# Performance work log

Hardware: AMD Instinct MI355X
Metric: run time of the kernel (lower is better)

The kernel has to match this reference:

```python
import jax, jax.numpy as jnp
import numpy as np
import math


def gen_slopes(n_heads, alibi_bias_max=1.0):
    # matches torch gen_slopes: _n_heads = next pow2, m = arange(1.._n)*max/_n, slopes = 2^-m
    _n = 2 ** math.ceil(math.log2(n_heads))
    m = jnp.arange(1, _n + 1, dtype=jnp.float32) * (alibi_bias_max / _n)
    slopes = 1.0 / jnp.power(2.0, m)
    if _n != n_heads:
        slopes = jnp.concatenate([slopes[1::2], slopes[::2]])[:n_heads]
    return slopes.reshape(1, n_heads, 1, 1)


def build_alibi_bias(n_heads, seq_len, alibi_bias_max=1.0):
    # full=False branch: bias over key positions only, shape [1, H, 1, L]
    pos = jnp.arange(1 - seq_len, 1, dtype=jnp.float32).reshape(1, 1, 1, seq_len)
    return pos * gen_slopes(n_heads, alibi_bias_max)


def setup_inputs() -> dict:
    key = jax.random.key(0)
    kq, kk, kv = jax.random.split(key, 3)
    B, L, H, E = 8, 1024, 8, 64
    return {
        "queries": jax.random.normal(kq, (B, L, H, E), dtype=jnp.float32),
        "keys": jax.random.normal(kk, (B, L, H, E), dtype=jnp.float32),
        "values": jax.random.normal(kv, (B, L, H, E), dtype=jnp.float32),
        "patch_index": -1,
    }


def reference(queries, keys, values, patch_index):
    B, L, H, E = queries.shape
    scale = 1.0 / math.sqrt(E)
    # scores: [B, H, L, L]
    scores = jnp.einsum('blhe,bshe->bhls', queries, keys)
    attn = scale * scores + build_alibi_bias(H, L)  # ALiBi bias, alibi_bias_max=1
    series = jax.nn.softmax(attn, axis=-1)  # dropout is identity in eval mode
    V = jnp.einsum('bhls,bshd->blhd', series, values)
    # patch_index == -1: identity branch, series unchanged
    return (V, series)
```

## Files before the change

kernel.cpp:

```cpp
#include <hip/hip_runtime.h>
#include <hip/hip_bf16.h>


typedef short short8 __attribute__((ext_vector_type(8)));
typedef short short4v __attribute__((ext_vector_type(4)));
typedef float f32x4 __attribute__((ext_vector_type(4)));
typedef unsigned short u16x4 __attribute__((ext_vector_type(4)));

#define B_ 8
#define L_ 1024
#define H_ 8
#define E_ 64
#define RSTRIDE (H_ * E_)
#define QBLK 64
#define CHUNK 64
#define NCH (L_ / CHUNK)
#define CHUNK_USH (CHUNK * E_)

__device__ __forceinline__ unsigned short f2bf(float f) {
  return __builtin_bit_cast(unsigned short, __float2bfloat16(f));
}
__device__ __forceinline__ short8 ldfrag(const float* p) {
  float4 a = *reinterpret_cast<const float4*>(p);
  float4 b = *reinterpret_cast<const float4*>(p + 4);
  return (short8){(short)f2bf(a.x), (short)f2bf(a.y), (short)f2bf(a.z),
                  (short)f2bf(a.w), (short)f2bf(b.x), (short)f2bf(b.y),
                  (short)f2bf(b.z), (short)f2bf(b.w)};
}

__device__ __forceinline__ f32x4 mfma16(short4v a, short4v b, f32x4 c) {
#if __has_builtin(__builtin_amdgcn_mfma_f32_16x16x16bf16_1k)
  return __builtin_amdgcn_mfma_f32_16x16x16bf16_1k(a, b, c, 0, 0, 0);
#else
  asm volatile(
      "s_nop 1\n\t"
      "v_mfma_f32_16x16x16_bf16 %0, %1, %2, %0\n\t"
      "s_nop 2"
      : "+v"(c)
      : "v"(a), "v"(b));
  return c;
#endif
}

__device__ __forceinline__ void gld16(const unsigned short* g,
                                      unsigned short* l) {
  __builtin_amdgcn_global_load_lds(
      (const __attribute__((address_space(1))) unsigned int*)g,
      (__attribute__((address_space(3))) unsigned int*)l, 16, 0, 0);
}

#define BAR_VM(N)                                         \
  {                                                       \
    asm volatile("s_waitcnt vmcnt(" #N ")" ::: "memory"); \
    __builtin_amdgcn_s_barrier();                         \
    __builtin_amdgcn_sched_barrier(0);                    \
  }

__global__ __launch_bounds__(256, 4) void prep_kv(
    const float* __restrict__ Kg, const float* __restrict__ Vg,
    unsigned short* __restrict__ Kbf, unsigned short* __restrict__ VTbf) {
  __shared__ unsigned short vt[64 * 64];

  const int t = threadIdx.x;
  const int id = blockIdx.x;
  const int bh = id & 63;
  const int sc = id >> 6;
  const int h = bh & 7, b = bh >> 3;
  const int s0 = sc * CHUNK;

  const float* Kb = Kg + ((size_t)b * L_ + s0) * RSTRIDE + h * E_;
  const float* Vb = Vg + ((size_t)b * L_ + s0) * RSTRIDE + h * E_;
  unsigned short* Ko = Kbf + (size_t)(bh * NCH + sc) * CHUNK_USH;
  unsigned short* Vo = VTbf + (size_t)(bh * NCH + sc) * CHUNK_USH;

#pragma unroll
  for (int i = 0; i < 2; ++i) {
    const int j = t + 256 * i;
    const int s = j >> 3;
    const int e8 = (j & 7) ^ (s & 7);
    const float* kp = Kb + (size_t)s * RSTRIDE + 8 * e8;
    float4 a = *reinterpret_cast<const float4*>(kp);
    float4 c = *reinterpret_cast<const float4*>(kp + 4);
    *reinterpret_cast<u16x4*>(&Ko[j * 8]) =
        (u16x4){f2bf(a.x), f2bf(a.y), f2bf(a.z), f2bf(a.w)};
    *reinterpret_cast<u16x4*>(&Ko[j * 8 + 4]) =
        (u16x4){f2bf(c.x), f2bf(c.y), f2bf(c.z), f2bf(c.w)};
  }
  {
    const int e = t & 63, w = t >> 6;
#pragma unroll
    for (int i = 0; i < 4; ++i) {
      const int s4 = 4 * w + 16 * i;
      const float* vp = Vb + (size_t)s4 * RSTRIDE + e;
      u16x4 u = {f2bf(vp[0]), f2bf(vp[RSTRIDE]), f2bf(vp[2 * RSTRIDE]),
                 f2bf(vp[3 * RSTRIDE])};
      *reinterpret_cast<u16x4*>(
          &vt[e * 64 + (((s4 >> 3) ^ (e & 7)) << 3) + (s4 & 7)]) = u;
    }
  }
  __syncthreads();
#pragma unroll
  for (int i = 0; i < 2; ++i) {
    const int j = t + 256 * i;
    u16x4 u0 = *reinterpret_cast<const u16x4*>(&vt[j * 8]);
    u16x4 u1 = *reinterpret_cast<const u16x4*>(&vt[j * 8 + 4]);
    *reinterpret_cast<u16x4*>(&Vo[j * 8]) = u0;
    *reinterpret_cast<u16x4*>(&Vo[j * 8 + 4]) = u1;
  }
}

__global__ __launch_bounds__(256, 4) void alibi_attn(
    const float* __restrict__ Qg, const unsigned short* __restrict__ Kbf,
    const unsigned short* __restrict__ VTbf, float* __restrict__ Vout,
    float* __restrict__ Pout) {
  __shared__ unsigned short sBuf[4][CHUNK_USH];

  const int t = threadIdx.x;
  const int lane = t & 63;
  const int w = t >> 6;
  const int col = lane & 15;
  const int kg = lane >> 4;

  const int id = blockIdx.x;
  const int qb = id >> 6;
  const int bh = id & 63;
  const int h = bh & 7;
  const int b = bh >> 3;
  const int q0 = qb * QBLK;

  const float sc_l2e = 0.125f * 1.44269504f;
  const float sl_l2e = exp2f(-(float)(h + 1) * 0.125f) * 1.44269504f;

  const unsigned short* Kc = Kbf + (size_t)bh * NCH * CHUNK_USH;
  const unsigned short* Vc = VTbf + (size_t)bh * NCH * CHUNK_USH;

  short8 qf0, qf1;
  {
    const float* qp =
        Qg + ((size_t)b * L_ + q0 + 16 * w + col) * RSTRIDE + h * E_ + 8 * kg;
    qf0 = ldfrag(qp);
    qf1 = ldfrag(qp + 32);
  }

  const float kbias0 = sl_l2e * (float)(4 * kg - 1023) - 32.0f;

#define STAGE(srcbase, c, dst)                                       \
  {                                                                  \
    const unsigned short* src = (srcbase) + (size_t)(c)*CHUNK_USH;   \
    _Pragma("unroll") for (int i = 0; i < 2; ++i) {                  \
      const int seg = i * 4 + w;                                     \
      gld16(src + (size_t)(seg * 64 + lane) * 8, (dst) + seg * 512); \
    }                                                                \
  }
#define PIN() __builtin_amdgcn_sched_barrier(0)

  float z0 = 0.f, z1 = 0.f, z2 = 0.f, z3 = 0.f;
  STAGE(Kc, 0, sBuf[0]);
  STAGE(Kc, 1, sBuf[1]);
  PIN();
  BAR_VM(2);
  for (int c = 0; c < NCH; ++c) {
    if (c + 2 < NCH) {
      STAGE(Kc, c + 2, sBuf[(c + 2) & 3]);
      PIN();
    }
    const unsigned short* kb = sBuf[c & 3];
#pragma unroll
    for (int kt = 0; kt < 4; ++kt) {
      const int row = 16 * kt + col;
      short8 k0 = *reinterpret_cast<const short8*>(
          &kb[row * 64 + ((kg ^ (row & 7)) << 3)]);
      short8 k1 = *reinterpret_cast<const short8*>(
          &kb[row * 64 + (((kg + 4) ^ (row & 7)) << 3)]);
      f32x4 acc = {0.f, 0.f, 0.f, 0.f};
      acc = __builtin_amdgcn_mfma_f32_16x16x32_bf16(k0, qf0, acc, 0, 0, 0);
      acc = __builtin_amdgcn_mfma_f32_16x16x32_bf16(k1, qf1, acc, 0, 0, 0);
      const float base = fmaf((float)(CHUNK * c + 16 * kt), sl_l2e, kbias0);
      z0 += __builtin_amdgcn_exp2f(fmaf(acc[0], sc_l2e, base));
      z1 += __builtin_amdgcn_exp2f(fmaf(acc[1], sc_l2e, base + sl_l2e));
      z2 += __builtin_amdgcn_exp2f(fmaf(acc[2], sc_l2e, base + 2.f * sl_l2e));
      z3 += __builtin_amdgcn_exp2f(fmaf(acc[3], sc_l2e, base + 3.f * sl_l2e));
    }
    if (c + 2 < NCH) {
      BAR_VM(2);
    } else {
      BAR_VM(0);
    }
  }
  float z = (z0 + z1) + (z2 + z3);
  z += __shfl_xor(z, 16, 64);
  z += __shfl_xor(z, 32, 64);
  const float minv = 1.0f / z;

  f32x4 oacc[4];
#pragma unroll
  for (int et = 0; et < 4; ++et) oacc[et] = (f32x4){0.f, 0.f, 0.f, 0.f};

  float* Pb =
      Pout + ((size_t)(b * H_ + h) * L_ + q0 + 16 * w + col) * L_ + 4 * kg;

  __syncthreads();
  STAGE(Kc, 0, sBuf[0]);
  STAGE(Vc, 0, sBuf[2]);
  PIN();
  BAR_VM(0);
  for (int c = 0; c < NCH; ++c) {
    if (c + 1 < NCH) {
      STAGE(Kc, c + 1, sBuf[(c + 1) & 1]);
      STAGE(Vc, c + 1, sBuf[2 + ((c + 1) & 1)]);
      PIN();
    }
    const unsigned short* kb = sBuf[c & 1];
    const unsigned short* vb = sBuf[2 + (c & 1)];
#pragma unroll
    for (int kt = 0; kt < 4; ++kt) {
      const int row = 16 * kt + col;
      short8 k0 = *reinterpret_cast<const short8*>(
          &kb[row * 64 + ((kg ^ (row & 7)) << 3)]);
      short8 k1 = *reinterpret_cast<const short8*>(
          &kb[row * 64 + (((kg + 4) ^ (row & 7)) << 3)]);
      f32x4 acc = {0.f, 0.f, 0.f, 0.f};
      acc = __builtin_amdgcn_mfma_f32_16x16x32_bf16(k0, qf0, acc, 0, 0, 0);
      acc = __builtin_amdgcn_mfma_f32_16x16x32_bf16(k1, qf1, acc, 0, 0, 0);
      short4v vf[4];
      const int g0 = 2 * kt + (kg >> 1);
      const int so = 4 * (kg & 1);
#pragma unroll
      for (int et = 0; et < 4; ++et) {
        const int e = 16 * et + col;
        vf[et] = *reinterpret_cast<const short4v*>(
            &vb[e * 64 + ((g0 ^ (e & 7)) << 3) + so]);
      }
      const float base = fmaf((float)(CHUNK * c + 16 * kt), sl_l2e, kbias0);
      f32x4 pf;
      pf[0] = __builtin_amdgcn_exp2f(fmaf(acc[0], sc_l2e, base)) * minv;
      pf[1] =
          __builtin_amdgcn_exp2f(fmaf(acc[1], sc_l2e, base + sl_l2e)) * minv;
      pf[2] = __builtin_amdgcn_exp2f(fmaf(acc[2], sc_l2e, base + 2.f * sl_l2e)) *
              minv;
      pf[3] = __builtin_amdgcn_exp2f(fmaf(acc[3], sc_l2e, base + 3.f * sl_l2e)) *
              minv;
      *reinterpret_cast<f32x4*>(Pb + CHUNK * c + 16 * kt) = pf;
      short4v pa = {(short)f2bf(pf[0]), (short)f2bf(pf[1]), (short)f2bf(pf[2]),
                    (short)f2bf(pf[3])};
#pragma unroll
      for (int et = 0; et < 4; ++et) oacc[et] = mfma16(pa, vf[et], oacc[et]);
    }
    BAR_VM(4);
  }

  float* Vo = Vout + (((size_t)b * L_ + q0 + 16 * w) * H_ + h) * E_;
#pragma unroll
  for (int et = 0; et < 4; ++et) {
#pragma unroll
    for (int r = 0; r < 4; ++r) {
      __builtin_nontemporal_store(oacc[et][r],
                                  &Vo[(4 * kg + r) * RSTRIDE + 16 * et + col]);
    }
  }
}

extern "C" void kernel_launch(void* const* d_in, const int* in_sizes, int n_in,
                              void* d_out, int out_size, void* d_ws,
                              size_t ws_size, hipStream_t stream) {
  const float* Q = (const float*)d_in[0];
  const float* K = (const float*)d_in[1];
  const float* V = (const float*)d_in[2];
  float* out = (float*)d_out;
  float* Vo = out;
  float* Po = out + (size_t)B_ * L_ * H_ * E_;
  unsigned short* Kbf = (unsigned short*)d_ws;
  unsigned short* VTbf = Kbf + (size_t)B_ * H_ * L_ * E_;
  hipLaunchKernelGGL(prep_kv, dim3(NCH * B_ * H_), dim3(256), 0, stream, K, V,
                     Kbf, VTbf);
  hipLaunchKernelGGL(alibi_attn, dim3((L_ / QBLK) * H_ * B_), dim3(256), 0,
                     stream, Q, Kbf, VTbf, Vo, Po);
}
```

Before: 95.36 us.

## Halve query block and key chunk size to two-wave workgroups

```diff
diff --git a/kernel.cpp b/kernel.cpp
--- a/kernel.cpp
+++ b/kernel.cpp
@@ -12,8 +12,8 @@
 #define H_ 8
 #define E_ 64
 #define RSTRIDE (H_ * E_)
-#define QBLK 64
-#define CHUNK 64
+#define QBLK 32
+#define CHUNK 32
 #define NCH (L_ / CHUNK)
 #define CHUNK_USH (CHUNK * E_)
 
@@ -55,47 +55,52 @@
     __builtin_amdgcn_s_barrier();                         \
     __builtin_amdgcn_sched_barrier(0);                    \
   }
+#define PIN() __builtin_amdgcn_sched_barrier(0)
 
 __global__ __launch_bounds__(256, 4) void prep_kv(
     const float* __restrict__ Kg, const float* __restrict__ Vg,
     unsigned short* __restrict__ Kbf, unsigned short* __restrict__ VTbf) {
-  __shared__ unsigned short vt[64 * 64];
+  __shared__ unsigned short vt[2 * CHUNK_USH];
 
   const int t = threadIdx.x;
   const int id = blockIdx.x;
   const int bh = id & 63;
   const int sc = id >> 6;
   const int h = bh & 7, b = bh >> 3;
-  const int s0 = sc * CHUNK;
+  const int s0 = sc * 64;
 
   const float* Kb = Kg + ((size_t)b * L_ + s0) * RSTRIDE + h * E_;
   const float* Vb = Vg + ((size_t)b * L_ + s0) * RSTRIDE + h * E_;
-  unsigned short* Ko = Kbf + (size_t)(bh * NCH + sc) * CHUNK_USH;
-  unsigned short* Vo = VTbf + (size_t)(bh * NCH + sc) * CHUNK_USH;
+  unsigned short* Ko = Kbf + (size_t)(bh * NCH + 2 * sc) * CHUNK_USH;
+  unsigned short* Vo = VTbf + (size_t)(bh * NCH + 2 * sc) * CHUNK_USH;
 
 #pragma unroll
   for (int i = 0; i < 2; ++i) {
     const int j = t + 256 * i;
-    const int s = j >> 3;
-    const int e8 = (j & 7) ^ (s & 7);
-    const float* kp = Kb + (size_t)s * RSTRIDE + 8 * e8;
+    const int ch = j >> 8;
+    const int jj = j & 255;
+    const int s = jj >> 3;
+    const int e8 = (jj & 7) ^ (s & 7);
+    const float* kp = Kb + (size_t)(32 * ch + s) * RSTRIDE + 8 * e8;
     float4 a = *reinterpret_cast<const float4*>(kp);
     float4 c = *reinterpret_cast<const float4*>(kp + 4);
-    *reinterpret_cast<u16x4*>(&Ko[j * 8]) =
+    *reinterpret_cast<u16x4*>(&Ko[(size_t)ch * CHUNK_USH + jj * 8]) =
         (u16x4){f2bf(a.x), f2bf(a.y), f2bf(a.z), f2bf(a.w)};
-    *reinterpret_cast<u16x4*>(&Ko[j * 8 + 4]) =
+    *reinterpret_cast<u16x4*>(&Ko[(size_t)ch * CHUNK_USH + jj * 8 + 4]) =
         (u16x4){f2bf(c.x), f2bf(c.y), f2bf(c.z), f2bf(c.w)};
   }
   {
-    const int e = t & 63, w = t >> 6;
+    const int e = t & 63, w4 = t >> 6;
 #pragma unroll
     for (int i = 0; i < 4; ++i) {
-      const int s4 = 4 * w + 16 * i;
+      const int s4 = 4 * w4 + 16 * i;
+      const int ch = s4 >> 5;
+      const int u = (s4 & 31) >> 2;
+      const int slot = u ^ (e & 7);
       const float* vp = Vb + (size_t)s4 * RSTRIDE + e;
-      u16x4 u = {f2bf(vp[0]), f2bf(vp[RSTRIDE]), f2bf(vp[2 * RSTRIDE]),
-                 f2bf(vp[3 * RSTRIDE])};
-      *reinterpret_cast<u16x4*>(
-          &vt[e * 64 + (((s4 >> 3) ^ (e & 7)) << 3) + (s4 & 7)]) = u;
+      u16x4 uv = {f2bf(vp[0]), f2bf(vp[RSTRIDE]), f2bf(vp[2 * RSTRIDE]),
+                  f2bf(vp[3 * RSTRIDE])};
+      *reinterpret_cast<u16x4*>(&vt[ch * CHUNK_USH + e * 32 + slot * 4]) = uv;
     }
   }
   __syncthreads();
@@ -109,7 +114,7 @@
   }
 }
 
-__global__ __launch_bounds__(256, 4) void alibi_attn(
+__global__ __launch_bounds__(128, 4) void alibi_attn(
     const float* __restrict__ Qg, const unsigned short* __restrict__ Kbf,
     const unsigned short* __restrict__ VTbf, float* __restrict__ Vout,
     float* __restrict__ Pout) {
@@ -148,11 +153,10 @@
   {                                                                  \
     const unsigned short* src = (srcbase) + (size_t)(c)*CHUNK_USH;   \
     _Pragma("unroll") for (int i = 0; i < 2; ++i) {                  \
-      const int seg = i * 4 + w;                                     \
+      const int seg = i * 2 + w;                                     \
       gld16(src + (size_t)(seg * 64 + lane) * 8, (dst) + seg * 512); \
     }                                                                \
   }
-#define PIN() __builtin_amdgcn_sched_barrier(0)
 
   float z0 = 0.f, z1 = 0.f, z2 = 0.f, z3 = 0.f;
   STAGE(Kc, 0, sBuf[0]);
@@ -166,7 +170,7 @@
     }
     const unsigned short* kb = sBuf[c & 3];
 #pragma unroll
-    for (int kt = 0; kt < 4; ++kt) {
+    for (int kt = 0; kt < 2; ++kt) {
       const int row = 16 * kt + col;
       short8 k0 = *reinterpret_cast<const short8*>(
           &kb[row * 64 + ((kg ^ (row & 7)) << 3)]);
@@ -213,7 +217,7 @@
     const unsigned short* kb = sBuf[c & 1];
     const unsigned short* vb = sBuf[2 + (c & 1)];
 #pragma unroll
-    for (int kt = 0; kt < 4; ++kt) {
+    for (int kt = 0; kt < 2; ++kt) {
       const int row = 16 * kt + col;
       short8 k0 = *reinterpret_cast<const short8*>(
           &kb[row * 64 + ((kg ^ (row & 7)) << 3)]);
@@ -223,13 +227,12 @@
       acc = __builtin_amdgcn_mfma_f32_16x16x32_bf16(k0, qf0, acc, 0, 0, 0);
       acc = __builtin_amdgcn_mfma_f32_16x16x32_bf16(k1, qf1, acc, 0, 0, 0);
       short4v vf[4];
-      const int g0 = 2 * kt + (kg >> 1);
-      const int so = 4 * (kg & 1);
 #pragma unroll
       for (int et = 0; et < 4; ++et) {
         const int e = 16 * et + col;
-        vf[et] = *reinterpret_cast<const short4v*>(
-            &vb[e * 64 + ((g0 ^ (e & 7)) << 3) + so]);
+        const int slot = (4 * kt + kg) ^ (e & 7);
+        vf[et] =
+            *reinterpret_cast<const short4v*>(&vb[e * 32 + slot * 4]);
       }
       const float base = fmaf((float)(CHUNK * c + 16 * kt), sl_l2e, kbias0);
       f32x4 pf;
@@ -246,7 +249,7 @@
 #pragma unroll
       for (int et = 0; et < 4; ++et) oacc[et] = mfma16(pa, vf[et], oacc[et]);
     }
-    BAR_VM(4);
+    BAR_VM(2);
   }
 
   float* Vo = Vout + (((size_t)b * L_ + q0 + 16 * w) * H_ + h) * E_;
@@ -271,8 +274,8 @@
   float* Po = out + (size_t)B_ * L_ * H_ * E_;
   unsigned short* Kbf = (unsigned short*)d_ws;
   unsigned short* VTbf = Kbf + (size_t)B_ * H_ * L_ * E_;
-  hipLaunchKernelGGL(prep_kv, dim3(NCH * B_ * H_), dim3(256), 0, stream, K, V,
+  hipLaunchKernelGGL(prep_kv, dim3(16 * B_ * H_), dim3(256), 0, stream, K, V,
                      Kbf, VTbf);
-  hipLaunchKernelGGL(alibi_attn, dim3((L_ / QBLK) * H_ * B_), dim3(256), 0,
+  hipLaunchKernelGGL(alibi_attn, dim3((L_ / QBLK) * H_ * B_), dim3(128), 0,
                      stream, Q, Kbf, VTbf, Vo, Po);
 }
```

Result: no change. 97.11 us (+1.8%).

## Fuse two-pass softmax into single pass with split-key waves and deferred normalization

Applied to the files above, without the earlier changes.

```diff
diff --git a/kernel.cpp b/kernel.cpp
--- a/kernel.cpp
+++ b/kernel.cpp
@@ -19,6 +19,9 @@
 
 __device__ __forceinline__ unsigned short f2bf(float f) {
   return __builtin_bit_cast(unsigned short, __float2bfloat16(f));
+}
+__device__ __forceinline__ float bf2f(unsigned int ubits) {
+  return __builtin_bit_cast(float, ubits << 16);
 }
 __device__ __forceinline__ short8 ldfrag(const float* p) {
   float4 a = *reinterpret_cast<const float4*>(p);
@@ -55,6 +58,7 @@
     __builtin_amdgcn_s_barrier();                         \
     __builtin_amdgcn_sched_barrier(0);                    \
   }
+#define PIN() __builtin_amdgcn_sched_barrier(0)
 
 __global__ __launch_bounds__(256, 4) void prep_kv(
     const float* __restrict__ Kg, const float* __restrict__ Vg,
@@ -109,15 +113,20 @@
   }
 }
 
-__global__ __launch_bounds__(256, 4) void alibi_attn(
+__global__ __launch_bounds__(512, 4) void alibi_attn(
     const float* __restrict__ Qg, const unsigned short* __restrict__ Kbf,
     const unsigned short* __restrict__ VTbf, float* __restrict__ Vout,
     float* __restrict__ Pout) {
-  __shared__ unsigned short sBuf[4][CHUNK_USH];
+  __shared__ unsigned short sK[2][2][CHUNK_USH];
+  __shared__ unsigned short sV[2][2][CHUNK_USH];
+  __shared__ float zbuf[2][4][16];
+  __shared__ float zinv[4][16];
 
   const int t = threadIdx.x;
   const int lane = t & 63;
   const int w = t >> 6;
+  const int qs = w & 3;
+  const int kh = w >> 2;
   const int col = lane & 15;
   const int kg = lane >> 4;
 
@@ -137,7 +146,7 @@
   short8 qf0, qf1;
   {
     const float* qp =
-        Qg + ((size_t)b * L_ + q0 + 16 * w + col) * RSTRIDE + h * E_ + 8 * kg;
+        Qg + ((size_t)b * L_ + q0 + 16 * qs + col) * RSTRIDE + h * E_ + 8 * kg;
     qf0 = ldfrag(qp);
     qf1 = ldfrag(qp + 32);
   }
@@ -148,23 +157,31 @@
   {                                                                  \
     const unsigned short* src = (srcbase) + (size_t)(c)*CHUNK_USH;   \
     _Pragma("unroll") for (int i = 0; i < 2; ++i) {                  \
-      const int seg = i * 4 + w;                                     \
+      const int seg = i * 4 + qs;                                    \
       gld16(src + (size_t)(seg * 64 + lane) * 8, (dst) + seg * 512); \
     }                                                                \
   }
-#define PIN() __builtin_amdgcn_sched_barrier(0)
-
-  float z0 = 0.f, z1 = 0.f, z2 = 0.f, z3 = 0.f;
-  STAGE(Kc, 0, sBuf[0]);
-  STAGE(Kc, 1, sBuf[1]);
+
+  float z0 = 0.f, z1 = 0.f;
+  f32x4 oacc[4];
+#pragma unroll
+  for (int et = 0; et < 4; ++et) oacc[et] = (f32x4){0.f, 0.f, 0.f, 0.f};
+  uint2 pw[8][4];
+
+  STAGE(Kc, 8 * kh, sK[kh][0]);
+  STAGE(Vc, 8 * kh, sV[kh][0]);
   PIN();
-  BAR_VM(2);
-  for (int c = 0; c < NCH; ++c) {
-    if (c + 2 < NCH) {
-      STAGE(Kc, c + 2, sBuf[(c + 2) & 3]);
+  BAR_VM(0);
+#pragma unroll
+  for (int c = 0; c < 8; ++c) {
+    if (c + 1 < 8) {
+      STAGE(Kc, 8 * kh + c + 1, sK[kh][(c + 1) & 1]);
+      STAGE(Vc, 8 * kh + c + 1, sV[kh][(c + 1) & 1]);
       PIN();
     }
-    const unsigned short* kb = sBuf[c & 3];
+    const int cc = 8 * kh + c;
+    const unsigned short* kb = sK[kh][c & 1];
+    const unsigned short* vb = sV[kh][c & 1];
 #pragma unroll
     for (int kt = 0; kt < 4; ++kt) {
       const int row = 16 * kt + col;
@@ -175,87 +192,83 @@
       f32x4 acc = {0.f, 0.f, 0.f, 0.f};
       acc = __builtin_amdgcn_mfma_f32_16x16x32_bf16(k0, qf0, acc, 0, 0, 0);
       acc = __builtin_amdgcn_mfma_f32_16x16x32_bf16(k1, qf1, acc, 0, 0, 0);
-      const float base = fmaf((float)(CHUNK * c + 16 * kt), sl_l2e, kbias0);
-      z0 += __builtin_amdgcn_exp2f(fmaf(acc[0], sc_l2e, base));
-      z1 += __builtin_amdgcn_exp2f(fmaf(acc[1], sc_l2e, base + sl_l2e));
-      z2 += __builtin_amdgcn_exp2f(fmaf(acc[2], sc_l2e, base + 2.f * sl_l2e));
-      z3 += __builtin_amdgcn_exp2f(fmaf(acc[3], sc_l2e, base + 3.f * sl_l2e));
-    }
-    if (c + 2 < NCH) {
-      BAR_VM(2);
-    } else {
-      BAR_VM(0);
-    }
-  }
-  float z = (z0 + z1) + (z2 + z3);
+      const float base = fmaf((float)(CHUNK * cc + 16 * kt), sl_l2e, kbias0);
+      float e0 = __builtin_amdgcn_exp2f(fmaf(acc[0], sc_l2e, base));
+      float e1 = __builtin_amdgcn_exp2f(fmaf(acc[1], sc_l2e, base + sl_l2e));
+      float e2 =
+          __builtin_amdgcn_exp2f(fmaf(acc[2], sc_l2e, base + 2.f * sl_l2e));
+      float e3 =
+          __builtin_amdgcn_exp2f(fmaf(acc[3], sc_l2e, base + 3.f * sl_l2e));
+      z0 += e0 + e1;
+      z1 += e2 + e3;
+      const unsigned int b0 = f2bf(e0), b1 = f2bf(e1);
+      const unsigned int b2 = f2bf(e2), b3 = f2bf(e3);
+      pw[c][kt] = make_uint2(b0 | (b1 << 16), b2 | (b3 << 16));
+      short4v pa = {(short)(unsigned short)b0, (short)(unsigned short)b1,
+                    (short)(unsigned short)b2, (short)(unsigned short)b3};
+#pragma unroll
+      for (int et = 0; et < 4; ++et) {
+        const int e = 16 * et + col;
+        const int g0 = 2 * kt + (kg >> 1);
+        short4v vf = *reinterpret_cast<const short4v*>(
+            &vb[e * 64 + ((g0 ^ (e & 7)) << 3) + 4 * (kg & 1)]);
+        oacc[et] = mfma16(pa, vf, oacc[et]);
+      }
+    }
+    BAR_VM(0);
+  }
+
+  float z = z0 + z1;
   z += __shfl_xor(z, 16, 64);
   z += __shfl_xor(z, 32, 64);
-  const float minv = 1.0f / z;
-
-  f32x4 oacc[4];
-#pragma unroll
-  for (int et = 0; et < 4; ++et) oacc[et] = (f32x4){0.f, 0.f, 0.f, 0.f};
-
-  float* Pb =
-      Pout + ((size_t)(b * H_ + h) * L_ + q0 + 16 * w + col) * L_ + 4 * kg;
-
+  if (kg == 0) zbuf[kh][qs][col] = z;
   __syncthreads();
-  STAGE(Kc, 0, sBuf[0]);
-  STAGE(Vc, 0, sBuf[2]);
-  PIN();
-  BAR_VM(0);
-  for (int c = 0; c < NCH; ++c) {
-    if (c + 1 < NCH) {
-      STAGE(Kc, c + 1, sBuf[(c + 1) & 1]);
-      STAGE(Vc, c + 1, sBuf[2 + ((c + 1) & 1)]);
-      PIN();
-    }
-    const unsigned short* kb = sBuf[c & 1];
-    const unsigned short* vb = sBuf[2 + (c & 1)];
+  const float minv = 1.0f / (zbuf[0][qs][col] + zbuf[1][qs][col]);
+
+  if (kh == 0 && kg == 0) zinv[qs][col] = minv;
+
+  float* obuf = reinterpret_cast<float*>(&sK[0][0][0]);
+  if (kh == 1) {
+#pragma unroll
+    for (int et = 0; et < 4; ++et)
+#pragma unroll
+      for (int r = 0; r < 4; ++r)
+        obuf[(qs * 16 + 4 * kg + r) * 64 + 16 * et + col] = oacc[et][r];
+  }
+  __syncthreads();
+  if (kh == 0) {
+    float minvR[4];
+#pragma unroll
+    for (int r = 0; r < 4; ++r) minvR[r] = zinv[qs][4 * kg + r];
+    float* Vo = Vout + (((size_t)b * L_ + q0 + 16 * qs) * H_ + h) * E_;
+#pragma unroll
+    for (int et = 0; et < 4; ++et) {
+#pragma unroll
+      for (int r = 0; r < 4; ++r) {
+        const float o =
+            (oacc[et][r] + obuf[(qs * 16 + 4 * kg + r) * 64 + 16 * et + col]) *
+            minvR[r];
+        __builtin_nontemporal_store(
+            o, &Vo[(4 * kg + r) * RSTRIDE + 16 * et + col]);
+      }
+    }
+  }
+
+  float* Pb = Pout + ((size_t)(b * H_ + h) * L_ + q0 + 16 * qs + col) * L_ +
+              4 * kg;
+#pragma unroll
+  for (int c = 0; c < 8; ++c) {
+    const int cc = 8 * kh + c;
 #pragma unroll
     for (int kt = 0; kt < 4; ++kt) {
-      const int row = 16 * kt + col;
-      short8 k0 = *reinterpret_cast<const short8*>(
-          &kb[row * 64 + ((kg ^ (row & 7)) << 3)]);
-      short8 k1 = *reinterpret_cast<const short8*>(
-          &kb[row * 64 + (((kg + 4) ^ (row & 7)) << 3)]);
-      f32x4 acc = {0.f, 0.f, 0.f, 0.f};
-      acc = __builtin_amdgcn_mfma_f32_16x16x32_bf16(k0, qf0, acc, 0, 0, 0);
-      acc = __builtin_amdgcn_mfma_f32_16x16x32_bf16(k1, qf1, acc, 0, 0, 0);
-      short4v vf[4];
-      const int g0 = 2 * kt + (kg >> 1);
-      const int so = 4 * (kg & 1);
-#pragma unroll
-      for (int et = 0; et < 4; ++et) {
-        const int e = 16 * et + col;
-        vf[et] = *reinterpret_cast<const short4v*>(
-            &vb[e * 64 + ((g0 ^ (e & 7)) << 3) + so]);
-      }
-      const float base = fmaf((float)(CHUNK * c + 16 * kt), sl_l2e, kbias0);
-      f32x4 pf;
-      pf[0] = __builtin_amdgcn_exp2f(fmaf(acc[0], sc_l2e, base)) * minv;
-      pf[1] =
-          __builtin_amdgcn_exp2f(fmaf(acc[1], sc_l2e, base + sl_l2e)) * minv;
-      pf[2] = __builtin_amdgcn_exp2f(fmaf(acc[2], sc_l2e, base + 2.f * sl_l2e)) *
-              minv;
-      pf[3] = __builtin_amdgcn_exp2f(fmaf(acc[3], sc_l2e, base + 3.f * sl_l2e)) *
-              minv;
-      *reinterpret_cast<f32x4*>(Pb + CHUNK * c + 16 * kt) = pf;
-      short4v pa = {(short)f2bf(pf[0]), (short)f2bf(pf[1]), (short)f2bf(pf[2]),
-                    (short)f2bf(pf[3])};
-#pragma unroll
-      for (int et = 0; et < 4; ++et) oacc[et] = mfma16(pa, vf[et], oacc[et]);
-    }
-    BAR_VM(4);
-  }
-
-  float* Vo = Vout + (((size_t)b * L_ + q0 + 16 * w) * H_ + h) * E_;
-#pragma unroll
-  for (int et = 0; et < 4; ++et) {
-#pragma unroll
-    for (int r = 0; r < 4; ++r) {
-      __builtin_nontemporal_store(oacc[et][r],
-                                  &Vo[(4 * kg + r) * RSTRIDE + 16 * et + col]);
+      const uint2 u = pw[c][kt];
+      f32x4 out;
+      out[0] = bf2f(u.x & 0xffffu) * minv;
+      out[1] = bf2f(u.x >> 16) * minv;
+      out[2] = bf2f(u.y & 0xffffu) * minv;
+      out[3] = bf2f(u.y >> 16) * minv;
+      __builtin_nontemporal_store(
+          out, reinterpret_cast<f32x4*>(Pb + CHUNK * cc + 16 * kt));
     }
   }
 }
@@ -273,6 +286,6 @@
   unsigned short* VTbf = Kbf + (size_t)B_ * H_ * L_ * E_;
   hipLaunchKernelGGL(prep_kv, dim3(NCH * B_ * H_), dim3(256), 0, stream, K, V,
                      Kbf, VTbf);
-  hipLaunchKernelGGL(alibi_attn, dim3((L_ / QBLK) * H_ * B_), dim3(256), 0,
+  hipLaunchKernelGGL(alibi_attn, dim3((L_ / QBLK) * H_ * B_), dim3(512), 0,
                      stream, Q, Kbf, VTbf, Vo, Po);
 }
```

Measured after the change: 127.1 us. 1.33x slower.

## Split softmax normalizer pass into separate split-K kernel with partial sums

Applied to the files above, without the earlier changes.

```diff
diff --git a/kernel.cpp b/kernel.cpp
--- a/kernel.cpp
+++ b/kernel.cpp
@@ -55,6 +55,7 @@
     __builtin_amdgcn_s_barrier();                         \
     __builtin_amdgcn_sched_barrier(0);                    \
   }
+#define PIN() __builtin_amdgcn_sched_barrier(0)
 
 __global__ __launch_bounds__(256, 4) void prep_kv(
     const float* __restrict__ Kg, const float* __restrict__ Vg,
@@ -109,11 +110,10 @@
   }
 }
 
-__global__ __launch_bounds__(256, 4) void alibi_attn(
+__global__ __launch_bounds__(256, 4) void z_pass(
     const float* __restrict__ Qg, const unsigned short* __restrict__ Kbf,
-    const unsigned short* __restrict__ VTbf, float* __restrict__ Vout,
-    float* __restrict__ Pout) {
-  __shared__ unsigned short sBuf[4][CHUNK_USH];
+    float* __restrict__ zp) {
+  __shared__ unsigned short sK[2][CHUNK_USH];
 
   const int t = threadIdx.x;
   const int lane = t & 63;
@@ -122,17 +122,19 @@
   const int kg = lane >> 4;
 
   const int id = blockIdx.x;
-  const int qb = id >> 6;
   const int bh = id & 63;
+  const int qk = id >> 6;
+  const int qb = qk >> 2;
+  const int ks = qk & 3;
   const int h = bh & 7;
   const int b = bh >> 3;
   const int q0 = qb * QBLK;
+  const int c0 = ks * 4;
 
   const float sc_l2e = 0.125f * 1.44269504f;
   const float sl_l2e = exp2f(-(float)(h + 1) * 0.125f) * 1.44269504f;
 
   const unsigned short* Kc = Kbf + (size_t)bh * NCH * CHUNK_USH;
-  const unsigned short* Vc = VTbf + (size_t)bh * NCH * CHUNK_USH;
 
   short8 qf0, qf1;
   {
@@ -141,30 +143,29 @@
     qf0 = ldfrag(qp);
     qf1 = ldfrag(qp + 32);
   }
-
   const float kbias0 = sl_l2e * (float)(4 * kg - 1023) - 32.0f;
 
-#define STAGE(srcbase, c, dst)                                       \
+#define STAGEZ(c, dst)                                               \
   {                                                                  \
-    const unsigned short* src = (srcbase) + (size_t)(c)*CHUNK_USH;   \
+    const unsigned short* src = Kc + (size_t)(c)*CHUNK_USH;          \
     _Pragma("unroll") for (int i = 0; i < 2; ++i) {                  \
       const int seg = i * 4 + w;                                     \
       gld16(src + (size_t)(seg * 64 + lane) * 8, (dst) + seg * 512); \
     }                                                                \
   }
-#define PIN() __builtin_amdgcn_sched_barrier(0)
 
   float z0 = 0.f, z1 = 0.f, z2 = 0.f, z3 = 0.f;
-  STAGE(Kc, 0, sBuf[0]);
-  STAGE(Kc, 1, sBuf[1]);
+  STAGEZ(c0, sK[0]);
   PIN();
-  BAR_VM(2);
-  for (int c = 0; c < NCH; ++c) {
-    if (c + 2 < NCH) {
-      STAGE(Kc, c + 2, sBuf[(c + 2) & 3]);
+  BAR_VM(0);
+#pragma unroll
+  for (int c = 0; c < 4; ++c) {
+    if (c + 1 < 4) {
+      STAGEZ(c0 + c + 1, sK[(c + 1) & 1]);
       PIN();
     }
-    const unsigned short* kb = sBuf[c & 3];
+    const int cc = c0 + c;
+    const unsigned short* kb = sK[c & 1];
 #pragma unroll
     for (int kt = 0; kt < 4; ++kt) {
       const int row = 16 * kt + col;
@@ -175,22 +176,62 @@
       f32x4 acc = {0.f, 0.f, 0.f, 0.f};
       acc = __builtin_amdgcn_mfma_f32_16x16x32_bf16(k0, qf0, acc, 0, 0, 0);
       acc = __builtin_amdgcn_mfma_f32_16x16x32_bf16(k1, qf1, acc, 0, 0, 0);
-      const float base = fmaf((float)(CHUNK * c + 16 * kt), sl_l2e, kbias0);
+      const float base = fmaf((float)(CHUNK * cc + 16 * kt), sl_l2e, kbias0);
       z0 += __builtin_amdgcn_exp2f(fmaf(acc[0], sc_l2e, base));
       z1 += __builtin_amdgcn_exp2f(fmaf(acc[1], sc_l2e, base + sl_l2e));
       z2 += __builtin_amdgcn_exp2f(fmaf(acc[2], sc_l2e, base + 2.f * sl_l2e));
       z3 += __builtin_amdgcn_exp2f(fmaf(acc[3], sc_l2e, base + 3.f * sl_l2e));
     }
-    if (c + 2 < NCH) {
-      BAR_VM(2);
-    } else {
-      BAR_VM(0);
-    }
+    BAR_VM(0);
   }
   float z = (z0 + z1) + (z2 + z3);
   z += __shfl_xor(z, 16, 64);
   z += __shfl_xor(z, 32, 64);
-  const float minv = 1.0f / z;
+  if (kg == 0) {
+    zp[(size_t)(ks * 64 + bh) * L_ + q0 + 16 * w + col] = z;
+  }
+}
+
+__global__ __launch_bounds__(256, 4) void p_pass(
+    const float* __restrict__ Qg, const unsigned short* __restrict__ Kbf,
+    const unsigned short* __restrict__ VTbf, const float* __restrict__ zp,
+    float* __restrict__ Vout, float* __restrict__ Pout) {
+  __shared__ unsigned short sBuf[4][CHUNK_USH];
+
+  const int t = threadIdx.x;
+  const int lane = t & 63;
+  const int w = t >> 6;
+  const int col = lane & 15;
+  const int kg = lane >> 4;
+
+  const int id = blockIdx.x;
+  const int qb = id >> 6;
+  const int bh = id & 63;
+  const int h = bh & 7;
+  const int b = bh >> 3;
+  const int q0 = qb * QBLK;
+
+  const float sc_l2e = 0.125f * 1.44269504f;
+  const float sl_l2e = exp2f(-(float)(h + 1) * 0.125f) * 1.44269504f;
+
+  const unsigned short* Kc = Kbf + (size_t)bh * NCH * CHUNK_USH;
+  const unsigned short* Vc = VTbf + (size_t)bh * NCH * CHUNK_USH;
+
+  short8 qf0, qf1;
+  {
+    const float* qp =
+        Qg + ((size_t)b * L_ + q0 + 16 * w + col) * RSTRIDE + h * E_ + 8 * kg;
+    qf0 = ldfrag(qp);
+    qf1 = ldfrag(qp + 32);
+  }
+  const float kbias0 = sl_l2e * (float)(4 * kg - 1023) - 32.0f;
+
+  float zsum;
+  {
+    const float* zb = zp + (size_t)bh * L_ + q0 + 16 * w + col;
+    zsum = zb[0] + zb[64 * L_] + zb[2 * 64 * L_] + zb[3 * 64 * L_];
+  }
+  const float minv = 1.0f / zsum;
 
   f32x4 oacc[4];
 #pragma unroll
@@ -199,7 +240,15 @@
   float* Pb =
       Pout + ((size_t)(b * H_ + h) * L_ + q0 + 16 * w + col) * L_ + 4 * kg;
 
-  __syncthreads();
+#define STAGE(srcbase, c, dst)                                       \
+  {                                                                  \
+    const unsigned short* src = (srcbase) + (size_t)(c)*CHUNK_USH;   \
+    _Pragma("unroll") for (int i = 0; i < 2; ++i) {                  \
+      const int seg = i * 4 + w;                                     \
+      gld16(src + (size_t)(seg * 64 + lane) * 8, (dst) + seg * 512); \
+    }                                                                \
+  }
+
   STAGE(Kc, 0, sBuf[0]);
   STAGE(Vc, 0, sBuf[2]);
   PIN();
@@ -254,8 +303,7 @@
   for (int et = 0; et < 4; ++et) {
 #pragma unroll
     for (int r = 0; r < 4; ++r) {
-      __builtin_nontemporal_store(oacc[et][r],
-                                  &Vo[(4 * kg + r) * RSTRIDE + 16 * et + col]);
+      Vo[(4 * kg + r) * RSTRIDE + 16 * et + col] = oacc[et][r];
     }
   }
 }
@@ -271,8 +319,11 @@
   float* Po = out + (size_t)B_ * L_ * H_ * E_;
   unsigned short* Kbf = (unsigned short*)d_ws;
   unsigned short* VTbf = Kbf + (size_t)B_ * H_ * L_ * E_;
+  float* zp = (float*)(VTbf + (size_t)B_ * H_ * L_ * E_);
   hipLaunchKernelGGL(prep_kv, dim3(NCH * B_ * H_), dim3(256), 0, stream, K, V,
                      Kbf, VTbf);
-  hipLaunchKernelGGL(alibi_attn, dim3((L_ / QBLK) * H_ * B_), dim3(256), 0,
-                     stream, Q, Kbf, VTbf, Vo, Po);
-}
+  hipLaunchKernelGGL(z_pass, dim3(16 * 4 * 64), dim3(256), 0, stream, Q, Kbf,
+                     zp);
+  hipLaunchKernelGGL(p_pass, dim3((L_ / QBLK) * H_ * B_), dim3(256), 0, stream,
+                     Q, Kbf, VTbf, zp, Vo, Po);
+}
```

New measurement: 105.0 us. 1.1x slower.
